# Optimization experiments

Hardware: AMD Instinct MI355X
Metric: run time of the kernel (lower is better)

Reference implementation:

```python
import jax, jax.numpy as jnp
import numpy as np

N = 4096      # nodes
F_IN = 512    # nfeat
D = 64        # nhid per head
H = 8         # nheads
C = 16        # nclass
K = 2         # k hops
ALPHA = 0.2   # leakyrelu slope
BETA = 0.9    # hop decay
NEG = jnp.float32(-9e15)


def _lrelu(v):
    return jnp.where(v > 0, v, ALPHA * v)


def setup_inputs() -> dict:
    key = jax.random.key(0)
    ks = jax.random.split(key, 8)
    x = jax.random.normal(ks[0], (N, F_IN), jnp.float32)
    # k-hop neighbor masks (dense, sparse-ish occupancy); self-loops kept so no row is fully masked
    masks = jax.random.bernoulli(ks[1], 0.01, (K, N, N))
    masks = masks | jnp.eye(N, dtype=bool)[None]
    W = jax.random.normal(ks[2], (H, F_IN, D), jnp.float32) * 0.05
    a1 = jax.random.normal(ks[3], (H, D), jnp.float32) * 0.05
    a2 = jax.random.normal(ks[4], (H, D), jnp.float32) * 0.05
    W_out = jax.random.normal(ks[5], (H * D, C), jnp.float32) * 0.05
    a_out1 = jax.random.normal(ks[6], (C,), jnp.float32) * 0.05
    a_out2 = jax.random.normal(ks[7], (C,), jnp.float32) * 0.05
    return dict(x=x, masks=masks, W=W, a1=a1, a2=a2, W_out=W_out, a_out1=a_out1, a_out2=a_out2)


def reference(x, masks, W, a1, a2, W_out, a_out1, a_out2):
    # ---- multi-head k-hop GAT layers (concat=True) ----
    Wh = jnp.einsum('nf,hfd->hnd', x, W)                      # [H,N,D]
    f1 = jnp.einsum('hnd,hd->hn', Wh, a1)                     # source term
    f2 = jnp.einsum('hnd,hd->hn', Wh, a2)                     # target term
    e = _lrelu(f1[:, :, None] + f2[:, None, :])               # [H,N,N]
    h = jnp.zeros_like(Wh)
    for hop in range(K):                                      # fixed small k
        att = jax.nn.softmax(jnp.where(masks[hop][None], e, NEG), axis=-1)
        h = h + (BETA ** hop) * jnp.einsum('hnm,hmd->hnd', att, Wh)
    h = jax.nn.elu(h)                                         # concat=True applies elu
    x2 = jnp.transpose(h, (1, 0, 2)).reshape(N, H * D)        # head concat

    # ---- output k-hop attention layer (concat=False) ----
    Who = x2 @ W_out                                          # [N,C]
    e2 = _lrelu((Who @ a_out1)[:, None] + (Who @ a_out2)[None, :])  # [N,N]
    out = jnp.zeros_like(Who)
    for hop in range(K):
        att = jax.nn.softmax(jnp.where(masks[hop], e2, NEG), axis=-1)
        out = out + (BETA ** hop) * (att @ Who)
    out = jax.nn.elu(out)
    return jax.nn.log_softmax(out, axis=1)
```

## Files before the change

### kernel.cpp

```cpp
#include <hip/hip_runtime.h>
#include <cstdint>

#define NN 4096
#define FIN 512
#define DD 64
#define HH 8
#define CC 16
#define KHOP 2
#define ALPHA 0.2f
#define BETA 0.9f

static __device__ __forceinline__ uint16_t f2bf(float f) {
    uint32_t u = __float_as_uint(f);
    u += 0x7FFFu + ((u >> 16) & 1u);
    return (uint16_t)(u >> 16);
}

static __device__ __forceinline__ uint32_t nz_nib(uint32_t x) {
    uint32_t zero80 = (x - 0x01010101u) & ~x & 0x80808080u;
    uint32_t nz80 = zero80 ^ 0x80808080u;
    return ((nz80 >> 7) * 0x01020408u) >> 24;
}

__global__ __launch_bounds__(256) void build_bits(const uint32_t* __restrict__ mraw,
                                                  uint64_t* __restrict__ bits) {
    const int totalWords = KHOP * NN * (NN / 64);
    const int tid = threadIdx.x;
    __shared__ int sflag;
    if (tid == 0) sflag = 1;
    __syncthreads();
    bool ok = true;
    for (int i = tid; i < 4096; i += 256) {
        uint32_t w = mraw[i];
        if (!(w == 0u || w == 1u || w == 0x3F800000u)) ok = false;
    }
    if (!ok) sflag = 0;
    __syncthreads();
    const int flag = sflag;

    const int wave_id = (blockIdx.x * 256 + tid) >> 6;
    const int lane = tid & 63;

    if (!flag) {
        const uint8_t* m8 = (const uint8_t*)mraw;
        const uint8_t* base = m8 + (size_t)wave_id * 8192 + (size_t)lane * 16;
        uint4 v[8];
#pragma unroll
        for (int i = 0; i < 8; ++i)
            v[i] = *(const uint4*)(base + (size_t)i * 1024);
        const int idx = (lane & 15) * 4;
#pragma unroll
        for (int i = 0; i < 8; ++i) {
            uint32_t m16 = nz_nib(v[i].x) | (nz_nib(v[i].y) << 4) |
                           (nz_nib(v[i].z) << 8) | (nz_nib(v[i].w) << 12);
            uint32_t u0 = (uint32_t)__shfl((int)m16, idx);
            uint32_t u1 = (uint32_t)__shfl((int)m16, idx + 1);
            uint32_t u2 = (uint32_t)__shfl((int)m16, idx + 2);
            uint32_t u3 = (uint32_t)__shfl((int)m16, idx + 3);
            if (lane < 16) {
                uint64_t wrd = (uint64_t)((u0 & 0xFFFFu) | (u1 << 16)) |
                               ((uint64_t)((u2 & 0xFFFFu) | (u3 << 16)) << 32);
                bits[(size_t)wave_id * 128 + i * 16 + lane] = wrd;
            }
        }
    } else {
        const int w0b = wave_id * 128;
        for (int w0 = w0b; w0 < w0b + 128 && w0 < totalWords; w0 += 8) {
            uint32_t v[8];
#pragma unroll
            for (int i = 0; i < 8; ++i)
                v[i] = mraw[(size_t)(w0 + i) * 64 + lane];
#pragma unroll
            for (int i = 0; i < 8; ++i) {
                unsigned long long b = __ballot(v[i] != 0u);
                if (lane == 0) bits[w0 + i] = b;
            }
        }
    }
}

__global__ __launch_bounds__(256) void wh_gemm(const float* __restrict__ x,
                                               const float* __restrict__ W,
                                               const float* __restrict__ a1,
                                               const float* __restrict__ a2,
                                               uint16_t* __restrict__ Whb,
                                               float* __restrict__ f1,
                                               float* __restrict__ f2) {
    const int h = blockIdx.y;
    const int n0 = blockIdx.x * 64;
    const int tid = threadIdx.x;
    const int d4 = (tid & 15) * 4;
    const int g = tid >> 4;
    const int nq = g * 4;
    __shared__ float xs[64 * 64];
    float acc[4][4] = {};
    const float* Wp = W + (size_t)h * FIN * DD;

    for (int fc = 0; fc < FIN; fc += 64) {
        {
            const int nl = tid >> 4;
            const int fl = (tid & 15) * 4;
#pragma unroll
            for (int r = 0; r < 4; ++r) {
                const int n = nl + r * 16;
                float4 xv = *(const float4*)&x[(size_t)(n0 + n) * FIN + fc + fl];
                const int ng = n >> 2, nb = n & 3;
                const float xe[4] = {xv.x, xv.y, xv.z, xv.w};
#pragma unroll
                for (int j = 0; j < 4; ++j) {
                    const int k = fl + j;
                    const int cg = ng ^ ((k + (k >> 2)) & 15);
                    xs[k * 64 + cg * 4 + nb] = xe[j];
                }
            }
        }
        __syncthreads();
#pragma unroll 4
        for (int k = 0; k < 64; ++k) {
            const int cg = g ^ ((k + (k >> 2)) & 15);
            float4 xv = *(const float4*)&xs[k * 64 + cg * 4];
            float4 wv = *(const float4*)&Wp[(size_t)(fc + k) * DD + d4];
            acc[0][0] += xv.x * wv.x; acc[0][1] += xv.x * wv.y; acc[0][2] += xv.x * wv.z; acc[0][3] += xv.x * wv.w;
            acc[1][0] += xv.y * wv.x; acc[1][1] += xv.y * wv.y; acc[1][2] += xv.y * wv.z; acc[1][3] += xv.y * wv.w;
            acc[2][0] += xv.z * wv.x; acc[2][1] += xv.z * wv.y; acc[2][2] += xv.z * wv.z; acc[2][3] += xv.z * wv.w;
            acc[3][0] += xv.w * wv.x; acc[3][1] += xv.w * wv.y; acc[3][2] += xv.w * wv.z; acc[3][3] += xv.w * wv.w;
        }
        __syncthreads();
    }

    const int nb0 = n0 + nq;
#pragma unroll
    for (int i = 0; i < 4; ++i) {
        ushort4 o;
        o.x = f2bf(acc[i][0]); o.y = f2bf(acc[i][1]);
        o.z = f2bf(acc[i][2]); o.w = f2bf(acc[i][3]);
        *(ushort4*)&Whb[((size_t)h * NN + nb0 + i) * DD + d4] = o;
    }
    float4 a1v = *(const float4*)&a1[h * DD + d4];
    float4 a2v = *(const float4*)&a2[h * DD + d4];
    float p1[4], p2[4];
#pragma unroll
    for (int i = 0; i < 4; ++i) {
        p1[i] = acc[i][0] * a1v.x + acc[i][1] * a1v.y + acc[i][2] * a1v.z + acc[i][3] * a1v.w;
        p2[i] = acc[i][0] * a2v.x + acc[i][1] * a2v.y + acc[i][2] * a2v.z + acc[i][3] * a2v.w;
#pragma unroll
        for (int off = 1; off < 16; off <<= 1) {
            p1[i] += __shfl_xor(p1[i], off);
            p2[i] += __shfl_xor(p2[i], off);
        }
    }
    if ((tid & 15) == 0) {
#pragma unroll
        for (int i = 0; i < 4; ++i) {
            f1[h * NN + nb0 + i] = p1[i];
            f2[h * NN + nb0 + i] = p2[i];
        }
    }
}

__global__ __launch_bounds__(512) void attn1(const uint64_t* __restrict__ bits,
                                             const uint16_t* __restrict__ Whb,
                                             const float* __restrict__ f1,
                                             const float* __restrict__ f2,
                                             const float* __restrict__ Wout,
                                             const float* __restrict__ ao1,
                                             const float* __restrict__ ao2,
                                             float* __restrict__ Who,
                                             float* __restrict__ g1,
                                             float* __restrict__ g2) {
    const int n = blockIdx.x;
    const int tid = threadIdx.x;
    const int h = tid >> 6, lane = tid & 63;
    const int hl = lane & 31, uh = lane >> 5;
    __shared__ uint16_t nbr[KHOP][NN];
    __shared__ float xrow[HH * DD];
    __shared__ float part[32][17];
    __shared__ int cnt[KHOP];
    if (h < KHOP) {
        const int hop = h;
        if (lane == 0) cnt[hop] = 0;
        uint64_t v = bits[((size_t)hop * NN + n) * 64 + lane];
        int c = __popcll(v);
        int base = 0;
        if (c) base = atomicAdd(&cnt[hop], c);
        int mb = lane * 64;
        while (v) {
            int j = __ffsll((unsigned long long)v) - 1;
            nbr[hop][base++] = (uint16_t)(mb + j);
            v &= v - 1;
        }
    }
    const float f1n = f1[h * NN + n];
    const float* __restrict__ f2h = f2 + h * NN;
    const char* gbase = (const char*)(Whb + (size_t)h * NN * DD) + hl * 4;
    __syncthreads();
    float res0 = 0.f, res1 = 0.f;
    for (int hop = 0; hop < KHOP; ++hop) {
        const int count = cnt[hop];
        const uint16_t* __restrict__ nb = nbr[hop];
        float acc0 = 0.f, acc1 = 0.f, denp = 0.f;
        for (int b0 = 0; b0 < count; b0 += 64) {
            const int bs = min(64, count - b0);
            uint32_t moff = 0u; float w = 0.f;
            if (lane < bs) {
                int m = nb[b0 + lane];
                float e = f1n + f2h[m];
                e = (e > 0.f) ? e : ALPHA * e;
                w = __expf(e);
                moff = (uint32_t)m << 7;
            }
            denp += w;
            const int nch = (bs + 15) >> 4;
            for (int c0 = 0; c0 < nch; ++c0) {
                const int jb = c0 << 4;
#pragma unroll
                for (int p = 0; p < 8; ++p) {
                    const int j = jb + 2 * p;
                    const uint32_t wu0 = __builtin_amdgcn_readlane(__float_as_uint(w), j);
                    const uint32_t wu1 = __builtin_amdgcn_readlane(__float_as_uint(w), j + 1);
                    const uint32_t o0 = __builtin_amdgcn_readlane(moff, j);
                    const uint32_t o1 = __builtin_amdgcn_readlane(moff, j + 1);
                    const float wsel = __uint_as_float(uh ? wu1 : wu0);
                    const uint32_t osel = uh ? o1 : o0;
                    const uint32_t dv = *(const uint32_t*)(gbase + osel);
                    acc0 += wsel * __uint_as_float(dv << 16);
                    acc1 += wsel * __uint_as_float(dv & 0xFFFF0000u);
                }
            }
        }
        float den = denp;
#pragma unroll
        for (int off = 1; off < 64; off <<= 1) den += __shfl_xor(den, off);
        acc0 += __shfl_xor(acc0, 32);
        acc1 += __shfl_xor(acc1, 32);
        const float scale = ((hop == 0) ? 1.f : BETA) / den;
        res0 += scale * acc0;
        res1 += scale * acc1;
    }
    float v0 = (res0 > 0.f) ? res0 : (__expf(res0) - 1.f);
    float v1 = (res1 > 0.f) ? res1 : (__expf(res1) - 1.f);
    if (uh == 0) {
        xrow[h * DD + 2 * hl]     = v0;
        xrow[h * DD + 2 * hl + 1] = v1;
    }
    __syncthreads();
    {
        const int c = tid & 15, chunk = tid >> 4;
        float p = 0.f;
#pragma unroll
        for (int i = 0; i < 16; ++i)
            p += xrow[chunk * 16 + i] * Wout[(chunk * 16 + i) * CC + c];
        part[chunk][c] = p;
    }
    __syncthreads();
    if (tid < 16) {
        float s = 0.f;
#pragma unroll
        for (int k = 0; k < 32; ++k) s += part[k][tid];
        Who[n * CC + tid] = s;
        float p1 = s * ao1[tid];
        float p2 = s * ao2[tid];
#pragma unroll
        for (int off = 1; off < 16; off <<= 1) {
            p1 += __shfl_xor(p1, off);
            p2 += __shfl_xor(p2, off);
        }
        if (tid == 0) { g1[n] = p1; g2[n] = p2; }
    }
}

__global__ __launch_bounds__(256) void attn2(const uint64_t* __restrict__ bits,
                                             const float* __restrict__ Who,
                                             const float* __restrict__ g1,
                                             const float* __restrict__ g2,
                                             float* __restrict__ out) {
    const int wv = threadIdx.x >> 6;
    const int lane = threadIdx.x & 63;
    const int n = blockIdx.x * 4 + wv;
    __shared__ uint16_t nbr[4][NN];
    uint16_t* mynbr = nbr[wv];
    const float g1n = g1[n];
    const int c = lane & 15, s = lane >> 4;
    float res = 0.f;
    for (int hop = 0; hop < KHOP; ++hop) {
        uint64_t v = bits[((size_t)hop * NN + n) * 64 + lane];
        int cpc = __popcll(v);
        int pref = cpc;
        for (int off = 1; off < 64; off <<= 1) {
            int t = __shfl_up(pref, off);
            if (lane >= off) pref += t;
        }
        int total = __shfl(pref, 63);
        int base = pref - cpc;
        int mb = lane * 64;
        while (v) {
            int j = __ffsll((unsigned long long)v) - 1;
            mynbr[base++] = (uint16_t)(mb + j);
            v &= v - 1;
        }
        __syncthreads();
        float acc = 0.f, den = 0.f;
        for (int j = s; j < total; j += 4) {
            int m = mynbr[j];
            float e = g1n + g2[m];
            e = (e > 0.f) ? e : ALPHA * e;
            float w = __expf(e);
            den += w;
            acc += w * Who[m * CC + c];
        }
        acc += __shfl_xor(acc, 16);
        acc += __shfl_xor(acc, 32);
        den += __shfl_xor(den, 16);
        den += __shfl_xor(den, 32);
        res += ((hop == 0) ? 1.f : BETA) * (acc / den);
        __syncthreads();
    }
    float o = (res > 0.f) ? res : (__expf(res) - 1.f);
    float mx = o;
    for (int off = 1; off < 16; off <<= 1) mx = fmaxf(mx, __shfl_xor(mx, off));
    float ex = __expf(o - mx);
    float sum = ex;
    for (int off = 1; off < 16; off <<= 1) sum += __shfl_xor(sum, off);
    float r = o - mx - __logf(sum);
    if (lane < 16) out[n * CC + c] = r;
}

extern "C" void kernel_launch(void* const* d_in, const int* in_sizes, int n_in,
                              void* d_out, int out_size, void* d_ws, size_t ws_size,
                              hipStream_t stream) {
    const float* x    = (const float*)d_in[0];
    const void*  masks= d_in[1];
    const float* W    = (const float*)d_in[2];
    const float* a1   = (const float*)d_in[3];
    const float* a2   = (const float*)d_in[4];
    const float* Wout = (const float*)d_in[5];
    const float* ao1  = (const float*)d_in[6];
    const float* ao2  = (const float*)d_in[7];
    float* out = (float*)d_out;

    char* ws = (char*)d_ws;
    uint64_t* bits = (uint64_t*)ws;
    uint16_t* Whb  = (uint16_t*)(ws + (size_t)KHOP * NN * 64 * 8);
    float* f1  = (float*)(Whb + (size_t)HH * NN * DD);
    float* f2  = f1 + (size_t)HH * NN;
    float* Who = f2 + (size_t)HH * NN;
    float* g1  = Who + (size_t)NN * CC;
    float* g2  = g1 + NN;

    build_bits<<<1024, 256, 0, stream>>>((const uint32_t*)masks, bits);
    wh_gemm<<<dim3(NN / 64, HH), 256, 0, stream>>>(x, W, a1, a2, Whb, f1, f2);
    attn1<<<NN, 512, 0, stream>>>(bits, Whb, f1, f2, Wout, ao1, ao2, Who, g1, g2);
    attn2<<<NN / 4, 256, 0, stream>>>(bits, Who, g1, g2, out);
    (void)in_sizes; (void)n_in; (void)out_size; (void)ws_size;
}
```

Baseline: 345.3 us.

## Use bf16 MFMA for Wh projection GEMM with pre-transposed bf16 weights

Adds a prep kernel that transposes W per head into bf16 [H,D,F] layout. wh_gemm then converts x tiles to bf16 in LDS and uses 16x16x32 bf16 MFMA instructions instead of the fp32 FMA outer-product loop, with the f1/f2 reductions adapted to the MFMA output layout. Separately, the second attention kernel drops its block barriers around the per-wave neighbor list and unrolls the gather loop by two. Inputs x and W now lose precision to bf16 before the GEMM, and relying on wave-local LDS ordering without barriers carries some race risk.

```diff
diff --git a/kernel.cpp b/kernel.cpp
--- a/kernel.cpp
+++ b/kernel.cpp
@@ -9,6 +9,9 @@
 #define KHOP 2
 #define ALPHA 0.2f
 #define BETA 0.9f
+
+typedef __attribute__((ext_vector_type(8))) short short8;
+typedef __attribute__((ext_vector_type(4))) float floatx4;
 
 static __device__ __forceinline__ uint16_t f2bf(float f) {
     uint32_t u = __float_as_uint(f);
@@ -79,8 +82,38 @@
     }
 }
 
+__global__ __launch_bounds__(256) void prep(const float* __restrict__ W,
+                                            uint16_t* __restrict__ Wt) {
+    const int h = blockIdx.y, kt = blockIdx.x;
+    const int t = threadIdx.x;
+    __shared__ float tile[64][65];
+    {
+        const int kr = t >> 4, d4 = (t & 15) * 4;
+#pragma unroll
+        for (int r = 0; r < 4; ++r) {
+            const int k = kr + r * 16;
+            float4 v = *(const float4*)&W[((size_t)h * FIN + kt * 64 + k) * DD + d4];
+            tile[k][d4 + 0] = v.x; tile[k][d4 + 1] = v.y;
+            tile[k][d4 + 2] = v.z; tile[k][d4 + 3] = v.w;
+        }
+    }
+    __syncthreads();
+    const int d = t >> 2, kb = (t & 3) * 16;
+    uint16_t tmp[16];
+#pragma unroll
+    for (int i = 0; i < 16; ++i) tmp[i] = f2bf(tile[kb + i][d]);
+    uint4 o0, o1;
+    o0.x = tmp[0] | ((uint32_t)tmp[1] << 16);  o0.y = tmp[2] | ((uint32_t)tmp[3] << 16);
+    o0.z = tmp[4] | ((uint32_t)tmp[5] << 16);  o0.w = tmp[6] | ((uint32_t)tmp[7] << 16);
+    o1.x = tmp[8] | ((uint32_t)tmp[9] << 16);  o1.y = tmp[10] | ((uint32_t)tmp[11] << 16);
+    o1.z = tmp[12] | ((uint32_t)tmp[13] << 16); o1.w = tmp[14] | ((uint32_t)tmp[15] << 16);
+    uint16_t* dst = Wt + ((size_t)h * DD + d) * FIN + kt * 64 + kb;
+    *(uint4*)dst = o0;
+    *(uint4*)(dst + 8) = o1;
+}
+
 __global__ __launch_bounds__(256) void wh_gemm(const float* __restrict__ x,
-                                               const float* __restrict__ W,
+                                               const uint16_t* __restrict__ Wt,
                                                const float* __restrict__ a1,
                                                const float* __restrict__ a2,
                                                uint16_t* __restrict__ Whb,
@@ -89,71 +122,77 @@
     const int h = blockIdx.y;
     const int n0 = blockIdx.x * 64;
     const int tid = threadIdx.x;
-    const int d4 = (tid & 15) * 4;
-    const int g = tid >> 4;
-    const int nq = g * 4;
-    __shared__ float xs[64 * 64];
-    float acc[4][4] = {};
-    const float* Wp = W + (size_t)h * FIN * DD;
-
-    for (int fc = 0; fc < FIN; fc += 64) {
+    const int wave = tid >> 6, lane = tid & 63;
+    const int q = lane >> 4, r = lane & 15;
+    __shared__ uint16_t xs[64 * 72];
+    __shared__ uint16_t ws[64 * 72];
+    floatx4 acc[4] = {floatx4{0,0,0,0}, floatx4{0,0,0,0}, floatx4{0,0,0,0}, floatx4{0,0,0,0}};
+
+    for (int chunk = 0; chunk < 8; ++chunk) {
+        const int fc = chunk * 64;
         {
-            const int nl = tid >> 4;
-            const int fl = (tid & 15) * 4;
-#pragma unroll
-            for (int r = 0; r < 4; ++r) {
-                const int n = nl + r * 16;
-                float4 xv = *(const float4*)&x[(size_t)(n0 + n) * FIN + fc + fl];
-                const int ng = n >> 2, nb = n & 3;
-                const float xe[4] = {xv.x, xv.y, xv.z, xv.w};
-#pragma unroll
-                for (int j = 0; j < 4; ++j) {
-                    const int k = fl + j;
-                    const int cg = ng ^ ((k + (k >> 2)) & 15);
-                    xs[k * 64 + cg * 4 + nb] = xe[j];
-                }
-            }
+            const int row = tid >> 4, c4 = (tid & 15) * 4;
+#pragma unroll
+            for (int rr = 0; rr < 4; ++rr) {
+                const int n = row + rr * 16;
+                float4 v = *(const float4*)&x[(size_t)(n0 + n) * FIN + fc + c4];
+                ushort4 o;
+                o.x = f2bf(v.x); o.y = f2bf(v.y); o.z = f2bf(v.z); o.w = f2bf(v.w);
+                *(ushort4*)&xs[n * 72 + c4] = o;
+            }
+            const int d = tid >> 2, kb = (tid & 3) * 16;
+            const uint16_t* src = Wt + ((size_t)h * DD + d) * FIN + fc + kb;
+            uint4 w0 = *(const uint4*)src;
+            uint4 w1 = *(const uint4*)(src + 8);
+            *(uint4*)&ws[d * 72 + kb] = w0;
+            *(uint4*)&ws[d * 72 + kb + 8] = w1;
         }
         __syncthreads();
-#pragma unroll 4
-        for (int k = 0; k < 64; ++k) {
-            const int cg = g ^ ((k + (k >> 2)) & 15);
-            float4 xv = *(const float4*)&xs[k * 64 + cg * 4];
-            float4 wv = *(const float4*)&Wp[(size_t)(fc + k) * DD + d4];
-            acc[0][0] += xv.x * wv.x; acc[0][1] += xv.x * wv.y; acc[0][2] += xv.x * wv.z; acc[0][3] += xv.x * wv.w;
-            acc[1][0] += xv.y * wv.x; acc[1][1] += xv.y * wv.y; acc[1][2] += xv.y * wv.z; acc[1][3] += xv.y * wv.w;
-            acc[2][0] += xv.z * wv.x; acc[2][1] += xv.z * wv.y; acc[2][2] += xv.z * wv.z; acc[2][3] += xv.z * wv.w;
-            acc[3][0] += xv.w * wv.x; acc[3][1] += xv.w * wv.y; acc[3][2] += xv.w * wv.z; acc[3][3] += xv.w * wv.w;
+        const int mrow = wave * 16 + r;
+        short8 a0 = *(const short8*)&xs[mrow * 72 + q * 8];
+        short8 a1f = *(const short8*)&xs[mrow * 72 + 32 + q * 8];
+#pragma unroll
+        for (int t = 0; t < 4; ++t) {
+            short8 b0 = *(const short8*)&ws[(t * 16 + r) * 72 + q * 8];
+            short8 b1 = *(const short8*)&ws[(t * 16 + r) * 72 + 32 + q * 8];
+            acc[t] = __builtin_amdgcn_mfma_f32_16x16x32_bf16(a0, b0, acc[t], 0, 0, 0);
+            acc[t] = __builtin_amdgcn_mfma_f32_16x16x32_bf16(a1f, b1, acc[t], 0, 0, 0);
         }
         __syncthreads();
     }
 
-    const int nb0 = n0 + nq;
-#pragma unroll
-    for (int i = 0; i < 4; ++i) {
-        ushort4 o;
-        o.x = f2bf(acc[i][0]); o.y = f2bf(acc[i][1]);
-        o.z = f2bf(acc[i][2]); o.w = f2bf(acc[i][3]);
-        *(ushort4*)&Whb[((size_t)h * NN + nb0 + i) * DD + d4] = o;
-    }
-    float4 a1v = *(const float4*)&a1[h * DD + d4];
-    float4 a2v = *(const float4*)&a2[h * DD + d4];
-    float p1[4], p2[4];
-#pragma unroll
-    for (int i = 0; i < 4; ++i) {
-        p1[i] = acc[i][0] * a1v.x + acc[i][1] * a1v.y + acc[i][2] * a1v.z + acc[i][3] * a1v.w;
-        p2[i] = acc[i][0] * a2v.x + acc[i][1] * a2v.y + acc[i][2] * a2v.z + acc[i][3] * a2v.w;
+#pragma unroll
+    for (int t = 0; t < 4; ++t) {
+#pragma unroll
+        for (int reg = 0; reg < 4; ++reg) {
+            const int m = wave * 16 + q * 4 + reg;
+            const int d = t * 16 + r;
+            Whb[((size_t)h * NN + n0 + m) * DD + d] = f2bf(acc[t][reg]);
+        }
+    }
+    float a1r[4], a2r[4];
+#pragma unroll
+    for (int t = 0; t < 4; ++t) {
+        a1r[t] = a1[h * DD + t * 16 + r];
+        a2r[t] = a2[h * DD + t * 16 + r];
+    }
+#pragma unroll
+    for (int reg = 0; reg < 4; ++reg) {
+        float p1 = 0.f, p2 = 0.f;
+#pragma unroll
+        for (int t = 0; t < 4; ++t) {
+            p1 += acc[t][reg] * a1r[t];
+            p2 += acc[t][reg] * a2r[t];
+        }
 #pragma unroll
         for (int off = 1; off < 16; off <<= 1) {
-            p1[i] += __shfl_xor(p1[i], off);
-            p2[i] += __shfl_xor(p2[i], off);
-        }
-    }
-    if ((tid & 15) == 0) {
-#pragma unroll
-        for (int i = 0; i < 4; ++i) {
-            f1[h * NN + nb0 + i] = p1[i];
-            f2[h * NN + nb0 + i] = p2[i];
+            p1 += __shfl_xor(p1, off);
+            p2 += __shfl_xor(p2, off);
+        }
+        if (r == 0) {
+            const int m = wave * 16 + q * 4 + reg;
+            f1[h * NN + n0 + m] = p1;
+            f2[h * NN + n0 + m] = p2;
         }
     }
 }
@@ -298,8 +337,8 @@
             mynbr[base++] = (uint16_t)(mb + j);
             v &= v - 1;
         }
-        __syncthreads();
         float acc = 0.f, den = 0.f;
+#pragma unroll 2
         for (int j = s; j < total; j += 4) {
             int m = mynbr[j];
             float e = g1n + g2[m];
@@ -313,7 +352,6 @@
         den += __shfl_xor(den, 16);
         den += __shfl_xor(den, 32);
         res += ((hop == 0) ? 1.f : BETA) * (acc / den);
-        __syncthreads();
     }
     float o = (res > 0.f) ? res : (__expf(res) - 1.f);
     float mx = o;
@@ -346,9 +384,11 @@
     float* Who = f2 + (size_t)HH * NN;
     float* g1  = Who + (size_t)NN * CC;
     float* g2  = g1 + NN;
+    uint16_t* Wt = (uint16_t*)(g2 + NN);
 
     build_bits<<<1024, 256, 0, stream>>>((const uint32_t*)masks, bits);
-    wh_gemm<<<dim3(NN / 64, HH), 256, 0, stream>>>(x, W, a1, a2, Whb, f1, f2);
+    prep<<<dim3(FIN / 64, HH), 256, 0, stream>>>(W, Wt);
+    wh_gemm<<<dim3(NN / 64, HH), 256, 0, stream>>>(x, Wt, a1, a2, Whb, f1, f2);
     attn1<<<NN, 512, 0, stream>>>(bits, Whb, f1, f2, Wout, ao1, ao2, Who, g1, g2);
     attn2<<<NN / 4, 256, 0, stream>>>(bits, Who, g1, g2, out);
     (void)in_sizes; (void)n_in; (void)out_size; (void)ws_size;
```

New measurement: 307.2 us. -11.0%, faster.
